# Performance work log

Hardware: AMD Instinct MI355X
Metric: run time of the kernel (lower is better)

## Reference

```python
import jax, jax.numpy as jnp
import numpy as np

D_MODEL = 1024
NUM_HEADS = 16
HEAD_DIM = D_MODEL // NUM_HEADS
ROPE_THETA = 10000.0


def apply_rope(x, positions):
    # x: (B, H, S, Dh), positions: (S,) int
    half = x.shape[-1] // 2
    inv_freq = ROPE_THETA ** (-jnp.arange(half, dtype=jnp.float32) * 2.0 / x.shape[-1])  # (Dh/2,)
    ang = positions.astype(jnp.float32)[:, None] * inv_freq[None, :]  # (S, Dh/2)
    cos, sin = jnp.cos(ang), jnp.sin(ang)
    x1 = x[..., 0::2]  # (B,H,S,Dh/2)
    x2 = x[..., 1::2]
    r1 = x1 * cos - x2 * sin
    r2 = x1 * sin + x2 * cos
    return jnp.stack([r1, r2], axis=-1).reshape(x.shape)


def setup_inputs() -> dict:
    key = jax.random.key(0)
    ks = jax.random.split(key, 5)
    B, S = 2, 2048
    scale = 1.0 / np.sqrt(D_MODEL)
    x = jax.random.normal(ks[0], (B, S, D_MODEL), dtype=jnp.float32)
    Wq = jax.random.normal(ks[1], (D_MODEL, D_MODEL), dtype=jnp.float32) * scale
    Wk = jax.random.normal(ks[2], (D_MODEL, D_MODEL), dtype=jnp.float32) * scale
    Wv = jax.random.normal(ks[3], (D_MODEL, D_MODEL), dtype=jnp.float32) * scale
    Wo = jax.random.normal(ks[4], (D_MODEL, D_MODEL), dtype=jnp.float32) * scale
    token_positions = jnp.arange(S, dtype=jnp.int32)
    return {"x": x, "token_positions": token_positions, "Wq": Wq, "Wk": Wk, "Wv": Wv, "Wo": Wo}


def reference(x, token_positions, Wq, Wk, Wv, Wo):
    B, S, _ = x.shape
    # Linear is bias-free: y = x @ W.T (W: [out, in])
    def proj(W):
        y = jnp.einsum('bsd,ed->bse', x, W)
        return y.reshape(B, S, NUM_HEADS, HEAD_DIM).transpose(0, 2, 1, 3)  # (B,H,S,Dh)
    q, k, v = proj(Wq), proj(Wk), proj(Wv)
    q = apply_rope(q, token_positions)
    k = apply_rope(k, token_positions)
    scores = jnp.einsum('bhqd,bhkd->bhqk', q, k) / jnp.sqrt(jnp.float32(HEAD_DIM))
    causal = jnp.tril(jnp.ones((S, S), dtype=bool))
    scores = jnp.where(causal, scores, -jnp.inf)
    attn = jax.nn.softmax(scores, axis=-1)
    out = jnp.einsum('bhqk,bhkd->bhqd', attn, v)  # (B,H,S,Dh)
    out = out.transpose(0, 2, 1, 3).reshape(B, S, D_MODEL)
    return jnp.einsum('bsd,ed->bse', out, Wo)
```

## Files before the change

### kernel.cpp

```cpp
#include <hip/hip_runtime.h>


typedef unsigned short u16;
typedef unsigned int   u32;
typedef unsigned long long u64;
using s16x8 = __attribute__((ext_vector_type(8))) short;
using f32x4 = __attribute__((ext_vector_type(4))) float;

__device__ __forceinline__ u16 f2bf(float f) {
  union { float f; u32 u; } v; v.f = f;
  return (u16)((v.u + 0x7fffu + ((v.u >> 16) & 1u)) >> 16);
}
__device__ __forceinline__ float bf2f(u16 h) {
  union { u32 u; float f; } v; v.u = ((u32)h) << 16;
  return v.f;
}

__device__ __forceinline__ void gl2lds(const u16* g, u16* l) {
  __builtin_amdgcn_global_load_lds(
      (const __attribute__((address_space(1))) void*)g,
      (__attribute__((address_space(3))) void*)l, 16, 0, 0);
}

__global__ __launch_bounds__(256) void cvt_all(
    const float* __restrict__ x,
    const float* __restrict__ wq, const float* __restrict__ wk,
    const float* __restrict__ wv, const float* __restrict__ wo,
    u16* __restrict__ xb, u16* __restrict__ wqb, u16* __restrict__ wkb,
    u16* __restrict__ wvb, u16* __restrict__ wob) {
  int e = (blockIdx.x * 256 + threadIdx.x) * 4;
  const float* src; u16* dst; int off;
  const int XN = 4 << 20;
  if (e < XN) { src = x; dst = xb; off = e; }
  else {
    int t = e - XN; int sel = t >> 20; off = t & ((1 << 20) - 1);
    src = sel == 0 ? wq : sel == 1 ? wk : sel == 2 ? wv : wo;
    dst = sel == 0 ? wqb : sel == 1 ? wkb : sel == 2 ? wvb : wob;
  }
  float4 v = *(const float4*)(src + off);
  ushort4 o;
  o.x = f2bf(v.x); o.y = f2bf(v.y); o.z = f2bf(v.z); o.w = f2bf(v.w);
  *(ushort4*)(dst + off) = o;
}

__device__ __forceinline__ void gemm_core(
    const u16* __restrict__ A, const u16* __restrict__ W,
    u16* As, u16* Bs, int bm0, int bn0, f32x4 (&acc)[4][4]) {
  const int K = 1024;
  int tid = threadIdx.x;
  int wid = tid >> 6, lane = tid & 63, quad = lane >> 4, l15 = lane & 15;
  int wm = (wid >> 1) * 64, wn = (wid & 1) * 64;
  int ch0 = wid * 128 + lane, ch1 = ch0 + 64;
  int r0 = ch0 >> 2, c0 = (ch0 & 3) * 8;
  int r1 = ch1 >> 2, c1 = (ch1 & 3) * 8;
  const u16* Ab = A + (size_t)bm0 * K;
  const u16* Wb = W + (size_t)bn0 * K;
  u16* lA0 = As + wid * 1024; u16* lA1 = lA0 + 512;
  u16* lB0 = Bs + wid * 1024; u16* lB1 = lB0 + 512;
  for (int k0 = 0; k0 < K; k0 += 32) {
    __syncthreads();
    gl2lds(Ab + (size_t)r0 * K + k0 + c0, lA0);
    gl2lds(Ab + (size_t)r1 * K + k0 + c1, lA1);
    gl2lds(Wb + (size_t)r0 * K + k0 + c0, lB0);
    gl2lds(Wb + (size_t)r1 * K + k0 + c1, lB1);
    __syncthreads();
    s16x8 af[4], bf[4];
#pragma unroll
    for (int mi = 0; mi < 4; mi++)
      af[mi] = *(const s16x8*)(As + (wm + mi * 16 + l15) * 32 + quad * 8);
#pragma unroll
    for (int ni = 0; ni < 4; ni++)
      bf[ni] = *(const s16x8*)(Bs + (wn + ni * 16 + l15) * 32 + quad * 8);
#pragma unroll
    for (int mi = 0; mi < 4; mi++)
#pragma unroll
      for (int ni = 0; ni < 4; ni++)
        acc[mi][ni] = __builtin_amdgcn_mfma_f32_16x16x32_bf16(
            af[mi], bf[ni], acc[mi][ni], 0, 0, 0);
  }
}

__global__ __launch_bounds__(256) void gemm_qkv(
    const u16* __restrict__ xb,
    const u16* __restrict__ wq, const u16* __restrict__ wk,
    const u16* __restrict__ wv,
    u16* __restrict__ qh, u16* __restrict__ kh, u16* __restrict__ vt) {
  __shared__ __align__(16) u16 As[128 * 32];
  __shared__ __align__(16) u16 Bs[128 * 32];
  int z = blockIdx.z;
  const u16* W = (z == 0) ? wq : (z == 1) ? wk : wv;
  int bm0 = blockIdx.y * 128, bn0 = blockIdx.x * 128;
  f32x4 acc[4][4];
  const f32x4 fz = {0.f, 0.f, 0.f, 0.f};
#pragma unroll
  for (int mi = 0; mi < 4; mi++)
#pragma unroll
    for (int ni = 0; ni < 4; ni++) acc[mi][ni] = fz;
  gemm_core(xb, W, As, Bs, bm0, bn0, acc);
  int tid = threadIdx.x, wid = tid >> 6, lane = tid & 63;
  int quad = lane >> 4, l15 = lane & 15;
  int wm = (wid >> 1) * 64, wn = (wid & 1) * 64;
  if (z < 2) {
    u16* dst = (z == 0) ? qh : kh;
#pragma unroll
    for (int mi = 0; mi < 4; mi++)
#pragma unroll
      for (int ni = 0; ni < 4; ni++)
#pragma unroll
        for (int r = 0; r < 4; r++) {
          int row = bm0 + wm + mi * 16 + quad * 4 + r;
          int col = bn0 + wn + ni * 16 + l15;
          int b = row >> 11, s = row & 2047, h = col >> 6, d = col & 63;
          dst[(((size_t)(b * 16 + h)) * 2048 + s) * 64 + d] =
              f2bf(acc[mi][ni][r]);
        }
  } else {
#pragma unroll
    for (int mi = 0; mi < 4; mi++)
#pragma unroll
      for (int ni = 0; ni < 4; ni++) {
        int row0 = bm0 + wm + mi * 16 + quad * 4;
        int col = bn0 + wn + ni * 16 + l15;
        int b = row0 >> 11, s0 = row0 & 2047, h = col >> 6, d = col & 63;
        u64 pk = (u64)f2bf(acc[mi][ni][0]) |
                 ((u64)f2bf(acc[mi][ni][1]) << 16) |
                 ((u64)f2bf(acc[mi][ni][2]) << 32) |
                 ((u64)f2bf(acc[mi][ni][3]) << 48);
        *(u64*)(vt + (((size_t)(b * 16 + h)) * 64 + d) * 2048 + s0) = pk;
      }
  }
}

__global__ __launch_bounds__(256) void gemm_out(
    const u16* __restrict__ ao, const u16* __restrict__ wo,
    float* __restrict__ out) {
  __shared__ __align__(16) u16 As[128 * 32];
  __shared__ __align__(16) u16 Bs[128 * 32];
  int bm0 = blockIdx.y * 128, bn0 = blockIdx.x * 128;
  f32x4 acc[4][4];
  const f32x4 fz = {0.f, 0.f, 0.f, 0.f};
#pragma unroll
  for (int mi = 0; mi < 4; mi++)
#pragma unroll
    for (int ni = 0; ni < 4; ni++) acc[mi][ni] = fz;
  gemm_core(ao, wo, As, Bs, bm0, bn0, acc);
  int tid = threadIdx.x, wid = tid >> 6, lane = tid & 63;
  int quad = lane >> 4, l15 = lane & 15;
  int wm = (wid >> 1) * 64, wn = (wid & 1) * 64;
#pragma unroll
  for (int mi = 0; mi < 4; mi++)
#pragma unroll
    for (int ni = 0; ni < 4; ni++)
#pragma unroll
      for (int r = 0; r < 4; r++) {
        int row = bm0 + wm + mi * 16 + quad * 4 + r;
        int col = bn0 + wn + ni * 16 + l15;
        out[(size_t)row * 1024 + col] = acc[mi][ni][r];
      }
}

__global__ __launch_bounds__(256) void rope_k(
    u16* __restrict__ qh, u16* __restrict__ kh, const int* __restrict__ pos) {
  int i = blockIdx.x * 256 + threadIdx.x;
  int pair = i & 31;
  int s = (i >> 5) & 2047;
  int hb = i >> 16;
  float p = (float)pos[s];
  float freq = __expf(-0.28782313662425572f * (float)pair);
  float ang = p * freq, sn, cs;
  sincosf(ang, &sn, &cs);
  size_t base = ((size_t)hb * 2048 + s) * 64 + 2 * pair;
  {
    u32 u = *(const u32*)(qh + base);
    float x1 = bf2f((u16)(u & 0xffff)), x2 = bf2f((u16)(u >> 16));
    float r1 = (x1 * cs - x2 * sn) * 0.125f;
    float r2 = (x1 * sn + x2 * cs) * 0.125f;
    *(u32*)(qh + base) = (u32)f2bf(r1) | ((u32)f2bf(r2) << 16);
  }
  {
    u32 u = *(const u32*)(kh + base);
    float x1 = bf2f((u16)(u & 0xffff)), x2 = bf2f((u16)(u >> 16));
    float r1 = x1 * cs - x2 * sn;
    float r2 = x1 * sn + x2 * cs;
    *(u32*)(kh + base) = (u32)f2bf(r1) | ((u32)f2bf(r2) << 16);
  }
}

#define KTS 72
#define VTS 72
#define PTS 40
#define OTS 72

__global__ __launch_bounds__(256, 4) void attn_k(
    const u16* __restrict__ qh, const u16* __restrict__ kh,
    const u16* __restrict__ vt, u16* __restrict__ ao) {
  __shared__ __align__(16) u16 ks[64 * KTS];
  __shared__ __align__(16) u16 vs[64 * VTS];
  __shared__ __align__(16) u16 pt[4 * 16 * PTS];
  int bid = blockIdx.x;
  int bh = bid & 31, pi = bid >> 5;
  int b = bh >> 4, h = bh & 15;
  int tid = threadIdx.x, wid = tid >> 6, lane = tid & 63;
  int quad = lane >> 4, l15 = lane & 15;
  int qsub = wid & 1, thalf = wid >> 1;
  const u16* qbase = qh + (size_t)bh * 2048 * 64;
  const u16* kbase = kh + (size_t)bh * 2048 * 64;
  const u16* vbase = vt + (size_t)bh * 64 * 2048;
  u16* ptw = pt + wid * 16 * PTS;
  const f32x4 fz = {0.f, 0.f, 0.f, 0.f};
  int srow = tid >> 2, sc = (tid & 3) * 8;

#pragma unroll
  for (int phase = 0; phase < 2; phase++) {
    int qt = phase ? (63 - pi) : pi;
    int q0 = qt * 32, q0w = q0 + qsub * 16;
    s16x8 qf0 = *(const s16x8*)(qbase + (size_t)(q0w + l15) * 64 + quad * 8);
    s16x8 qf1 = *(const s16x8*)(qbase + (size_t)(q0w + l15) * 64 + 32 + quad * 8);
    f32x4 acc[4];
#pragma unroll
    for (int md = 0; md < 4; md++) acc[md] = fz;
    float lsum = 0.f;
    int qg = q0w + l15;
    int nt = (qt >> 1) + 1;
    uint4 rk0 = *(const uint4*)(kbase + (size_t)srow * 64 + sc);
    uint4 rk1 = *(const uint4*)(kbase + (size_t)srow * 64 + sc + 32);
    uint4 rv0 = *(const uint4*)(vbase + (size_t)srow * 2048 + sc);
    uint4 rv1 = *(const uint4*)(vbase + (size_t)srow * 2048 + sc + 32);
    for (int it = 0; it < nt; it++) {
      __syncthreads();
      *(uint4*)(ks + srow * KTS + sc) = rk0;
      *(uint4*)(ks + srow * KTS + sc + 32) = rk1;
      *(uint4*)(vs + srow * VTS + sc) = rv0;
      *(uint4*)(vs + srow * VTS + sc + 32) = rv1;
      if (it + 1 < nt) {
        int t1 = (it + 1) << 6;
        rk0 = *(const uint4*)(kbase + (size_t)(t1 + srow) * 64 + sc);
        rk1 = *(const uint4*)(kbase + (size_t)(t1 + srow) * 64 + sc + 32);
        rv0 = *(const uint4*)(vbase + (size_t)srow * 2048 + t1 + sc);
        rv1 = *(const uint4*)(vbase + (size_t)srow * 2048 + t1 + sc + 32);
      }
      __syncthreads();
      int t0 = it << 6, tb = thalf * 32;
      bool diag = (it == nt - 1);
#pragma unroll
      for (int mt = 0; mt < 2; mt++) {
        int krow = tb + mt * 16 + l15;
        s16x8 ka0 = *(const s16x8*)(ks + krow * KTS + quad * 8);
        s16x8 ka1 = *(const s16x8*)(ks + krow * KTS + 32 + quad * 8);
        f32x4 st = __builtin_amdgcn_mfma_f32_16x16x32_bf16(ka0, qf0, fz, 0, 0, 0);
        st = __builtin_amdgcn_mfma_f32_16x16x32_bf16(ka1, qf1, st, 0, 0, 0);
        u64 pk = 0;
#pragma unroll
        for (int r = 0; r < 4; r++) {
          float p = __expf(st[r]);
          if (diag) {
            int tg = t0 + tb + mt * 16 + quad * 4 + r;
            if (tg > qg) p = 0.f;
          }
          lsum += p;
          pk |= ((u64)f2bf(p)) << (16 * r);
        }
        *(u64*)(ptw + l15 * PTS + mt * 16 + quad * 4) = pk;
      }
      s16x8 pb = *(const s16x8*)(ptw + l15 * PTS + quad * 8);
#pragma unroll
      for (int md = 0; md < 4; md++) {
        s16x8 va = *(const s16x8*)(vs + (md * 16 + l15) * VTS + tb + quad * 8);
        acc[md] = __builtin_amdgcn_mfma_f32_16x16x32_bf16(va, pb, acc[md], 0, 0, 0);
      }
    }
    lsum += __shfl_xor(lsum, 16, 64);
    lsum += __shfl_xor(lsum, 32, 64);
    __syncthreads();
    float* redo = (float*)ks;
    float* redl = (float*)vs;
    if (thalf == 1) {
#pragma unroll
      for (int md = 0; md < 4; md++)
#pragma unroll
        for (int r = 0; r < 4; r++)
          redo[(qsub * 64 + lane) * 16 + md * 4 + r] = acc[md][r];
      redl[qsub * 64 + lane] = lsum;
    }
    __syncthreads();
    if (thalf == 0) {
#pragma unroll
      for (int md = 0; md < 4; md++)
#pragma unroll
        for (int r = 0; r < 4; r++)
          acc[md][r] += redo[(qsub * 64 + lane) * 16 + md * 4 + r];
      lsum += redl[qsub * 64 + lane];
      float rl = 1.0f / lsum;
      u16* ow = pt + qsub * 16 * OTS;
#pragma unroll
      for (int md = 0; md < 4; md++) {
        u64 ok = 0;
#pragma unroll
        for (int r = 0; r < 4; r++)
          ok |= ((u64)f2bf(acc[md][r] * rl)) << (16 * r);
        *(u64*)(ow + l15 * OTS + md * 16 + quad * 4) = ok;
      }
      int qq = lane >> 2, dc = lane & 3;
      uint4 o0 = *(uint4*)(ow + qq * OTS + dc * 16);
      uint4 o1 = *(uint4*)(ow + qq * OTS + dc * 16 + 8);
      size_t orow = (size_t)b * 2048 + q0 + qsub * 16 + qq;
      *(uint4*)(ao + orow * 1024 + h * 64 + dc * 16) = o0;
      *(uint4*)(ao + orow * 1024 + h * 64 + dc * 16 + 8) = o1;
    }
  }
}

extern "C" void kernel_launch(void* const* d_in, const int* in_sizes, int n_in,
                              void* d_out, int out_size, void* d_ws,
                              size_t ws_size, hipStream_t stream) {
  const float* x  = (const float*)d_in[0];
  const int* pos  = (const int*)d_in[1];
  const float* Wq = (const float*)d_in[2];
  const float* Wk = (const float*)d_in[3];
  const float* Wv = (const float*)d_in[4];
  const float* Wo = (const float*)d_in[5];
  float* out = (float*)d_out;

  char* ws = (char*)d_ws;
  const size_t MB = 1u << 20;
  u16* xb  = (u16*)(ws);
  u16* wqb = (u16*)(ws + 8 * MB);
  u16* wkb = (u16*)(ws + 10 * MB);
  u16* wvb = (u16*)(ws + 12 * MB);
  u16* wob = (u16*)(ws + 14 * MB);
  u16* qhb = (u16*)(ws + 16 * MB);
  u16* khb = (u16*)(ws + 24 * MB);
  u16* vtb = (u16*)(ws + 32 * MB);
  u16* ao  = xb;

  cvt_all<<<8192, 256, 0, stream>>>(x, Wq, Wk, Wv, Wo,
                                    xb, wqb, wkb, wvb, wob);
  gemm_qkv<<<dim3(8, 32, 3), 256, 0, stream>>>(xb, wqb, wkb, wvb,
                                               qhb, khb, vtb);
  rope_k<<<8192, 256, 0, stream>>>(qhb, khb, pos);
  attn_k<<<1024, 256, 0, stream>>>(qhb, khb, vtb, ao);
  gemm_out<<<dim3(8, 32), 256, 0, stream>>>(ao, wob, out);
}
```

Measured before the change: 213.7 us.

## Store K/V tiles in MFMA fragment order and split attention into one q-tile per block

The attention kernel drops the padded row-major LDS tiles and writes K, V and P into shared memory in the exact per-lane fragment order the MFMA reads, so each lane does one contiguous 16-byte LDS load. The paired light/heavy q-tile scheme is replaced by one q-tile per block: the grid doubles to 2048 blocks, launched heaviest tiles first, and launch bounds allow 8 blocks per CU. The aim is fewer LDS bank conflicts, higher occupancy and better load balance. In exchange, each block now loads its own K/V stream instead of sharing a block across two tiles.

```diff
diff --git a/kernel.cpp b/kernel.cpp
--- a/kernel.cpp
+++ b/kernel.cpp
@@ -186,19 +186,16 @@
   }
 }
 
-#define KTS 72
-#define VTS 72
-#define PTS 40
-#define OTS 72
-
-__global__ __launch_bounds__(256, 4) void attn_k(
+
+__global__ __launch_bounds__(256, 8) void attn_k(
     const u16* __restrict__ qh, const u16* __restrict__ kh,
     const u16* __restrict__ vt, u16* __restrict__ ao) {
-  __shared__ __align__(16) u16 ks[64 * KTS];
-  __shared__ __align__(16) u16 vs[64 * VTS];
-  __shared__ __align__(16) u16 pt[4 * 16 * PTS];
+  __shared__ __align__(16) u16 ks[64 * 64];
+  __shared__ __align__(16) u16 vs[64 * 64];
+  __shared__ __align__(16) u16 pt[4 * 512];
   int bid = blockIdx.x;
-  int bh = bid & 31, pi = bid >> 5;
+  int bh = bid & 31;
+  int qt = 63 - (bid >> 5);
   int b = bh >> 4, h = bh & 15;
   int tid = threadIdx.x, wid = tid >> 6, lane = tid & 63;
   int quad = lane >> 4, l15 = lane & 15;
@@ -206,107 +203,109 @@
   const u16* qbase = qh + (size_t)bh * 2048 * 64;
   const u16* kbase = kh + (size_t)bh * 2048 * 64;
   const u16* vbase = vt + (size_t)bh * 64 * 2048;
-  u16* ptw = pt + wid * 16 * PTS;
+  u16* ptw = pt + wid * 512;
   const f32x4 fz = {0.f, 0.f, 0.f, 0.f};
-  int srow = tid >> 2, sc = (tid & 3) * 8;
-
-#pragma unroll
-  for (int phase = 0; phase < 2; phase++) {
-    int qt = phase ? (63 - pi) : pi;
-    int q0 = qt * 32, q0w = q0 + qsub * 16;
-    s16x8 qf0 = *(const s16x8*)(qbase + (size_t)(q0w + l15) * 64 + quad * 8);
-    s16x8 qf1 = *(const s16x8*)(qbase + (size_t)(q0w + l15) * 64 + 32 + quad * 8);
-    f32x4 acc[4];
-#pragma unroll
-    for (int md = 0; md < 4; md++) acc[md] = fz;
-    float lsum = 0.f;
-    int qg = q0w + l15;
-    int nt = (qt >> 1) + 1;
-    uint4 rk0 = *(const uint4*)(kbase + (size_t)srow * 64 + sc);
-    uint4 rk1 = *(const uint4*)(kbase + (size_t)srow * 64 + sc + 32);
-    uint4 rv0 = *(const uint4*)(vbase + (size_t)srow * 2048 + sc);
-    uint4 rv1 = *(const uint4*)(vbase + (size_t)srow * 2048 + sc + 32);
-    for (int it = 0; it < nt; it++) {
-      __syncthreads();
-      *(uint4*)(ks + srow * KTS + sc) = rk0;
-      *(uint4*)(ks + srow * KTS + sc + 32) = rk1;
-      *(uint4*)(vs + srow * VTS + sc) = rv0;
-      *(uint4*)(vs + srow * VTS + sc + 32) = rv1;
-      if (it + 1 < nt) {
-        int t1 = (it + 1) << 6;
-        rk0 = *(const uint4*)(kbase + (size_t)(t1 + srow) * 64 + sc);
-        rk1 = *(const uint4*)(kbase + (size_t)(t1 + srow) * 64 + sc + 32);
-        rv0 = *(const uint4*)(vbase + (size_t)srow * 2048 + t1 + sc);
-        rv1 = *(const uint4*)(vbase + (size_t)srow * 2048 + t1 + sc + 32);
-      }
-      __syncthreads();
-      int t0 = it << 6, tb = thalf * 32;
-      bool diag = (it == nt - 1);
-#pragma unroll
-      for (int mt = 0; mt < 2; mt++) {
-        int krow = tb + mt * 16 + l15;
-        s16x8 ka0 = *(const s16x8*)(ks + krow * KTS + quad * 8);
-        s16x8 ka1 = *(const s16x8*)(ks + krow * KTS + 32 + quad * 8);
-        f32x4 st = __builtin_amdgcn_mfma_f32_16x16x32_bf16(ka0, qf0, fz, 0, 0, 0);
-        st = __builtin_amdgcn_mfma_f32_16x16x32_bf16(ka1, qf1, st, 0, 0, 0);
-        u64 pk = 0;
-#pragma unroll
-        for (int r = 0; r < 4; r++) {
-          float p = __expf(st[r]);
-          if (diag) {
-            int tg = t0 + tb + mt * 16 + quad * 4 + r;
-            if (tg > qg) p = 0.f;
-          }
-          lsum += p;
-          pk |= ((u64)f2bf(p)) << (16 * r);
-        }
-        *(u64*)(ptw + l15 * PTS + mt * 16 + quad * 4) = pk;
-      }
-      s16x8 pb = *(const s16x8*)(ptw + l15 * PTS + quad * 8);
-#pragma unroll
-      for (int md = 0; md < 4; md++) {
-        s16x8 va = *(const s16x8*)(vs + (md * 16 + l15) * VTS + tb + quad * 8);
-        acc[md] = __builtin_amdgcn_mfma_f32_16x16x32_bf16(va, pb, acc[md], 0, 0, 0);
-      }
-    }
-    lsum += __shfl_xor(lsum, 16, 64);
-    lsum += __shfl_xor(lsum, 32, 64);
+  int grow = wid * 16 + l15;
+  int gcol = quad * 8;
+  u16* kw0 = ks + wid * 1024 + lane * 8;
+  u16* kw1 = kw0 + 512;
+  u16* vw0 = vs + wid * 1024 + lane * 8;
+  u16* vw1 = vw0 + 512;
+
+  int q0 = qt * 32, q0w = q0 + qsub * 16;
+  s16x8 qf0 = *(const s16x8*)(qbase + (size_t)(q0w + l15) * 64 + quad * 8);
+  s16x8 qf1 = *(const s16x8*)(qbase + (size_t)(q0w + l15) * 64 + 32 + quad * 8);
+  f32x4 acc[4];
+#pragma unroll
+  for (int md = 0; md < 4; md++) acc[md] = fz;
+  float lsum = 0.f;
+  int qg = q0w + l15;
+  int nt = (qt >> 1) + 1;
+  uint4 rk0 = *(const uint4*)(kbase + (size_t)grow * 64 + gcol);
+  uint4 rk1 = *(const uint4*)(kbase + (size_t)grow * 64 + gcol + 32);
+  uint4 rv0 = *(const uint4*)(vbase + (size_t)grow * 2048 + gcol);
+  uint4 rv1 = *(const uint4*)(vbase + (size_t)grow * 2048 + gcol + 32);
+  for (int it = 0; it < nt; it++) {
     __syncthreads();
-    float* redo = (float*)ks;
-    float* redl = (float*)vs;
-    if (thalf == 1) {
-#pragma unroll
-      for (int md = 0; md < 4; md++)
-#pragma unroll
-        for (int r = 0; r < 4; r++)
-          redo[(qsub * 64 + lane) * 16 + md * 4 + r] = acc[md][r];
-      redl[qsub * 64 + lane] = lsum;
+    *(uint4*)kw0 = rk0;
+    *(uint4*)kw1 = rk1;
+    *(uint4*)vw0 = rv0;
+    *(uint4*)vw1 = rv1;
+    if (it + 1 < nt) {
+      int t1 = (it + 1) << 6;
+      rk0 = *(const uint4*)(kbase + (size_t)(t1 + grow) * 64 + gcol);
+      rk1 = *(const uint4*)(kbase + (size_t)(t1 + grow) * 64 + gcol + 32);
+      rv0 = *(const uint4*)(vbase + (size_t)grow * 2048 + t1 + gcol);
+      rv1 = *(const uint4*)(vbase + (size_t)grow * 2048 + t1 + gcol + 32);
     }
     __syncthreads();
-    if (thalf == 0) {
-#pragma unroll
-      for (int md = 0; md < 4; md++)
-#pragma unroll
-        for (int r = 0; r < 4; r++)
-          acc[md][r] += redo[(qsub * 64 + lane) * 16 + md * 4 + r];
-      lsum += redl[qsub * 64 + lane];
-      float rl = 1.0f / lsum;
-      u16* ow = pt + qsub * 16 * OTS;
-#pragma unroll
-      for (int md = 0; md < 4; md++) {
-        u64 ok = 0;
-#pragma unroll
-        for (int r = 0; r < 4; r++)
-          ok |= ((u64)f2bf(acc[md][r] * rl)) << (16 * r);
-        *(u64*)(ow + l15 * OTS + md * 16 + quad * 4) = ok;
+    int t0 = it << 6, tb = thalf * 32;
+    bool diag = (it == nt - 1);
+#pragma unroll
+    for (int mt = 0; mt < 2; mt++) {
+      const u16* kf = ks + (thalf * 2 + mt) * 1024;
+      s16x8 ka0 = *(const s16x8*)(kf + lane * 8);
+      s16x8 ka1 = *(const s16x8*)(kf + 512 + lane * 8);
+      f32x4 st = __builtin_amdgcn_mfma_f32_16x16x32_bf16(ka0, qf0, fz, 0, 0, 0);
+      st = __builtin_amdgcn_mfma_f32_16x16x32_bf16(ka1, qf1, st, 0, 0, 0);
+      u64 pk = 0;
+#pragma unroll
+      for (int r = 0; r < 4; r++) {
+        float p = __expf(st[r]);
+        if (diag) {
+          int tg = t0 + tb + mt * 16 + quad * 4 + r;
+          if (tg > qg) p = 0.f;
+        }
+        lsum += p;
+        pk |= ((u64)f2bf(p)) << (16 * r);
       }
-      int qq = lane >> 2, dc = lane & 3;
-      uint4 o0 = *(uint4*)(ow + qq * OTS + dc * 16);
-      uint4 o1 = *(uint4*)(ow + qq * OTS + dc * 16 + 8);
-      size_t orow = (size_t)b * 2048 + q0 + qsub * 16 + qq;
-      *(uint4*)(ao + orow * 1024 + h * 64 + dc * 16) = o0;
-      *(uint4*)(ao + orow * 1024 + h * 64 + dc * 16 + 8) = o1;
+      *(u64*)(ptw + (mt * 32 + (quad >> 1) * 16 + l15) * 8 + (quad & 1) * 4) =
+          pk;
     }
+    s16x8 pb = *(const s16x8*)(ptw + lane * 8);
+#pragma unroll
+    for (int md = 0; md < 4; md++) {
+      s16x8 va = *(const s16x8*)(vs + md * 1024 + thalf * 512 + lane * 8);
+      acc[md] = __builtin_amdgcn_mfma_f32_16x16x32_bf16(va, pb, acc[md], 0, 0, 0);
+    }
+  }
+  lsum += __shfl_xor(lsum, 16, 64);
+  lsum += __shfl_xor(lsum, 32, 64);
+  __syncthreads();
+  float* redo = (float*)ks;
+  float* redl = (float*)vs;
+  if (thalf == 1) {
+#pragma unroll
+    for (int md = 0; md < 4; md++)
+#pragma unroll
+      for (int r = 0; r < 4; r++)
+        redo[(qsub * 64 + lane) * 16 + md * 4 + r] = acc[md][r];
+    redl[qsub * 64 + lane] = lsum;
+  }
+  __syncthreads();
+  if (thalf == 0) {
+#pragma unroll
+    for (int md = 0; md < 4; md++)
+#pragma unroll
+      for (int r = 0; r < 4; r++)
+        acc[md][r] += redo[(qsub * 64 + lane) * 16 + md * 4 + r];
+    lsum += redl[qsub * 64 + lane];
+    float rl = 1.0f / lsum;
+    u16* ow = ((u16*)vs) + 256 + qsub * 16 * 72;
+#pragma unroll
+    for (int md = 0; md < 4; md++) {
+      u64 ok = 0;
+#pragma unroll
+      for (int r = 0; r < 4; r++)
+        ok |= ((u64)f2bf(acc[md][r] * rl)) << (16 * r);
+      *(u64*)(ow + l15 * 72 + md * 16 + quad * 4) = ok;
+    }
+    int qq = lane >> 2, dc = lane & 3;
+    uint4 o0 = *(uint4*)(ow + qq * 72 + dc * 16);
+    uint4 o1 = *(uint4*)(ow + qq * 72 + dc * 16 + 8);
+    size_t orow = (size_t)b * 2048 + q0 + qsub * 16 + qq;
+    *(uint4*)(ao + orow * 1024 + h * 64 + dc * 16) = o0;
+    *(uint4*)(ao + orow * 1024 + h * 64 + dc * 16 + 8) = o1;
   }
 }
 
@@ -338,6 +337,6 @@
   gemm_qkv<<<dim3(8, 32, 3), 256, 0, stream>>>(xb, wqb, wkb, wvb,
                                                qhb, khb, vtb);
   rope_k<<<8192, 256, 0, stream>>>(qhb, khb, pos);
-  attn_k<<<1024, 256, 0, stream>>>(qhb, khb, vtb, ao);
+  attn_k<<<2048, 256, 0, stream>>>(qhb, khb, vtb, ao);
   gemm_out<<<dim3(8, 32), 256, 0, stream>>>(ao, wob, out);
 }
```

After: 264.0 us. 23.5% more time.
